# Performance work log

Measured on AMD Instinct MI355X. Metric: run time of the kernel, lower is better.

## Reference

```python
import jax, jax.numpy as jnp
import numpy as np

HEADS = 64
VOCAB = 5
EPS = 1e-5

def _layer_norm(x, g, b):
    mu = jnp.mean(x, axis=-1, keepdims=True)
    var = jnp.var(x, axis=-1, keepdims=True)
    return (x - mu) * jax.lax.rsqrt(var + EPS) * g + b

def setup_inputs() -> dict:
    key = jax.random.key(0)
    ks = jax.random.split(key, 12)
    h = HEADS
    s = 1.0 / np.sqrt(h)
    return {
        "x": jax.random.normal(ks[0], (8, 384, 384, h), dtype=jnp.float32),
        "W1": jax.random.normal(ks[1], (h, h), dtype=jnp.float32) * s,
        "b1": jnp.zeros((h,), jnp.float32),
        "W2": jax.random.normal(ks[2], (h, h), dtype=jnp.float32) * s,
        "b2": jnp.zeros((h,), jnp.float32),
        "W3": jax.random.normal(ks[3], (h, h), dtype=jnp.float32) * s,
        "b3": jnp.zeros((h,), jnp.float32),
        "ln_g": jnp.ones((h,), jnp.float32),
        "ln_b": jnp.zeros((h,), jnp.float32),
        "Wo": jax.random.normal(ks[4], (h, VOCAB), dtype=jnp.float32) * s,
        "bo": jnp.zeros((VOCAB,), jnp.float32),
    }

def reference(x, W1, b1, W2, b2, W3, b3, ln_g, ln_b, Wo, bo):
    # three (Linear -> gelu -> shared LayerNorm) blocks on [b,s,s,h]
    h = _layer_norm(jax.nn.gelu(x @ W1 + b1, approximate=False), ln_g, ln_b)
    h = _layer_norm(jax.nn.gelu(h @ W2 + b2, approximate=False), ln_g, ln_b)
    h = _layer_norm(jax.nn.gelu(h @ W3 + b3, approximate=False), ln_g, ln_b)
    out = h @ Wo + bo  # [b,s,s,vocab]
    return (out + jnp.swapaxes(out, 1, 2)) * 0.5
```

## Files before the change

### kernel.cpp

```cpp
#include <hip/hip_runtime.h>
#include <cstdint>
#include <cstddef>

typedef __attribute__((ext_vector_type(8))) __bf16   bf16x8;
typedef __attribute__((ext_vector_type(2))) __bf16   bf16x2;
typedef __attribute__((ext_vector_type(4))) float    f32x4;
typedef __attribute__((ext_vector_type(4))) uint32_t u32x4;
typedef __attribute__((ext_vector_type(2))) uint32_t u32x2;

#define N_ROWS   1179648
#define N_TILES  73728
#define BLOCKS   1024
#define TPW      18
#define SDIM     384
#define VOCAB    5

__device__ __forceinline__ float gelu_fast(float x){
  float u = x * x;
  float w = __builtin_fmaf(-0.10294456f, u, -2.3021255f);
  float e = __builtin_amdgcn_exp2f(x * w);
  return x * __builtin_amdgcn_rcpf(e + 1.0f);
}

__device__ __forceinline__ bf16x8 mk_bf8(f32x4 a, f32x4 b){
  bf16x8 v;
  v[0]=(__bf16)a[0]; v[1]=(__bf16)a[1]; v[2]=(__bf16)a[2]; v[3]=(__bf16)a[3];
  v[4]=(__bf16)b[0]; v[5]=(__bf16)b[1]; v[6]=(__bf16)b[2]; v[7]=(__bf16)b[3];
  return v;
}

__global__ __launch_bounds__(256)
void mlp_kernel(const float* __restrict__ x,
                const float* __restrict__ W1, const float* __restrict__ b1,
                const float* __restrict__ W2, const float* __restrict__ b2,
                const float* __restrict__ W3, const float* __restrict__ b3,
                const float* __restrict__ lng, const float* __restrict__ lnb,
                const float* __restrict__ Wo,  const float* __restrict__ bo,
                float* __restrict__ tmp)
{
  __shared__ __align__(16) uint8_t  Wl[27392];
  __shared__ __align__(16) uint32_t bounce[4][512];

  const int tid = threadIdx.x;

  {
    int m = tid & 63, g = tid >> 6;
    #pragma unroll 1
    for (int idx = g; idx < 96; idx += 4) {
      int L = idx >> 5, kp = idx & 31;
      const float* W = (L == 0) ? W1 : ((L == 1) ? W2 : W3);
      float lo = W[(2 * kp    ) * 64 + m];
      float hi = W[(2 * kp + 1) * 64 + m];
      bf16x2 p = { (__bf16)lo, (__bf16)hi };
      *(uint32_t*)(Wl + L * 8192 + m * 128 + ((4 * kp) ^ ((m & 7) << 4))) =
          __builtin_bit_cast(uint32_t, p);
    }
    int mm = tid & 15;
    #pragma unroll 1
    for (int kp = tid >> 4; kp < 32; kp += 16) {
      float lo = (mm < VOCAB) ? Wo[(2 * kp    ) * VOCAB + mm] : 0.0f;
      float hi = (mm < VOCAB) ? Wo[(2 * kp + 1) * VOCAB + mm] : 0.0f;
      bf16x2 p = { (__bf16)lo, (__bf16)hi };
      *(uint32_t*)(Wl + 24576 + mm * 128 + ((4 * kp) ^ ((mm & 7) << 4))) =
          __builtin_bit_cast(uint32_t, p);
    }
    if (tid < 192) {
      float v = (tid < 64) ? b1[tid] : ((tid < 128) ? b2[tid - 64] : b3[tid - 128]);
      *(float*)(Wl + 26624 + tid * 4) = v;
    }
  }
  __syncthreads();

  const int wav  = tid >> 6, lane = tid & 63;
  const int h    = lane >> 4;
  const int b    = lane & 15;
  const int swzW = (b & 7) << 4;
  const int swzD = (b & 7) << 2;
  const int rowB = b * 128;
  const int kOff = 16 * h;
  uint32_t* myB = bounce[wav];
  float*    myF = (float*)bounce[wav];
  const float* biasL = (const float*)(Wl + 26624);

  f32x4 ggr[4], bbr[4], aoInit;
  #pragma unroll
  for (int mt = 0; mt < 4; ++mt) {
    ggr[mt] = *(const f32x4*)(lng + 16 * mt + 4 * h);
    bbr[mt] = *(const f32x4*)(lnb + 16 * mt + 4 * h);
  }
  #pragma unroll
  for (int r = 0; r < 4; ++r) {
    int v = 4 * h + r;
    aoInit[r] = (v < VOCAB) ? bo[v] : 0.0f;
  }

  const int gw = blockIdx.x * 4 + wav;
  int t = gw * TPW;

  f32x4 xr[4];
  {
    const float* px = x + (size_t)(t * 16 + b) * 64 + 8 * h;
    xr[0] = *(const f32x4*)(px);
    xr[1] = *(const f32x4*)(px + 4);
    xr[2] = *(const f32x4*)(px + 32);
    xr[3] = *(const f32x4*)(px + 36);
  }

  #pragma unroll 1
  for (int i = 0; i < TPW; ++i, ++t) {
    f32x4 xn[4];
    {
      int tn = (t + 1 < N_TILES) ? (t + 1) : t;
      const float* pn = x + (size_t)(tn * 16 + b) * 64 + 8 * h;
      xn[0] = *(const f32x4*)(pn);
      xn[1] = *(const f32x4*)(pn + 4);
      xn[2] = *(const f32x4*)(pn + 32);
      xn[3] = *(const f32x4*)(pn + 36);
    }

    u32x4 bfr[2];
    bfr[0] = __builtin_bit_cast(u32x4, mk_bf8(xr[0], xr[1]));
    bfr[1] = __builtin_bit_cast(u32x4, mk_bf8(xr[2], xr[3]));

    #pragma unroll
    for (int L = 0; L < 3; ++L) {
      const uint8_t* wp = Wl + L * 8192 + rowB;
      f32x4 acc[4];
      #pragma unroll
      for (int mt = 0; mt < 4; ++mt) {
        u32x4 w0 = *(const u32x4*)(wp + mt * 2048 + ((kOff     ) ^ swzW));
        u32x4 w1 = *(const u32x4*)(wp + mt * 2048 + ((kOff + 64) ^ swzW));
        acc[mt] = *(const f32x4*)(biasL + L * 64 + 16 * mt + 4 * h);
        acc[mt] = __builtin_amdgcn_mfma_f32_16x16x32_bf16(
            __builtin_bit_cast(bf16x8, w0), __builtin_bit_cast(bf16x8, bfr[0]),
            acc[mt], 0, 0, 0);
        acc[mt] = __builtin_amdgcn_mfma_f32_16x16x32_bf16(
            __builtin_bit_cast(bf16x8, w1), __builtin_bit_cast(bf16x8, bfr[1]),
            acc[mt], 0, 0, 0);
      }

      #pragma unroll
      for (int mt = 0; mt < 4; ++mt)
        #pragma unroll
        for (int r = 0; r < 4; ++r)
          acc[mt][r] = gelu_fast(acc[mt][r]);

      float s1 = 0.0f, s2 = 0.0f;
      #pragma unroll
      for (int mt = 0; mt < 4; ++mt)
        #pragma unroll
        for (int r = 0; r < 4; ++r) {
          float v = acc[mt][r];
          s1 += v;
          s2 = __builtin_fmaf(v, v, s2);
        }
      s1 += __shfl_xor(s1, 16); s2 += __shfl_xor(s2, 16);
      s1 += __shfl_xor(s1, 32); s2 += __shfl_xor(s2, 32);
      float mu   = s1 * (1.0f / 64.0f);
      float var  = __builtin_fmaf(s2, (1.0f / 64.0f), -mu * mu);
      float rstd = rsqrtf(var + 1e-5f);
      float nm   = -mu * rstd;

      #pragma unroll
      for (int mt = 0; mt < 4; ++mt) {
        float n0 = __builtin_fmaf(__builtin_fmaf(acc[mt][0], rstd, nm), ggr[mt][0], bbr[mt][0]);
        float n1 = __builtin_fmaf(__builtin_fmaf(acc[mt][1], rstd, nm), ggr[mt][1], bbr[mt][1]);
        float n2 = __builtin_fmaf(__builtin_fmaf(acc[mt][2], rstd, nm), ggr[mt][2], bbr[mt][2]);
        float n3 = __builtin_fmaf(__builtin_fmaf(acc[mt][3], rstd, nm), ggr[mt][3], bbr[mt][3]);
        bf16x2 p0 = { (__bf16)n0, (__bf16)n1 };
        bf16x2 p1 = { (__bf16)n2, (__bf16)n3 };
        u32x2 pw = { __builtin_bit_cast(uint32_t, p0), __builtin_bit_cast(uint32_t, p1) };
        int di = (b * 32 + 8 * mt + 2 * h) ^ swzD;
        *(u32x2*)(myB + di) = pw;
      }
      #pragma unroll
      for (int s = 0; s < 2; ++s)
        bfr[s] = *(const u32x4*)(myB + ((b * 32 + 16 * s + 4 * h) ^ swzD));
    }

    f32x4 ao = aoInit;
    {
      const uint8_t* wp = Wl + 24576 + rowB;
      u32x4 w0 = *(const u32x4*)(wp + ((kOff     ) ^ swzW));
      u32x4 w1 = *(const u32x4*)(wp + ((kOff + 64) ^ swzW));
      ao = __builtin_amdgcn_mfma_f32_16x16x32_bf16(
          __builtin_bit_cast(bf16x8, w0), __builtin_bit_cast(bf16x8, bfr[0]),
          ao, 0, 0, 0);
      ao = __builtin_amdgcn_mfma_f32_16x16x32_bf16(
          __builtin_bit_cast(bf16x8, w1), __builtin_bit_cast(bf16x8, bfr[1]),
          ao, 0, 0, 0);
    }

    #pragma unroll
    for (int r = 0; r < 4; ++r) {
      int v = 4 * h + r;
      if (v < VOCAB) myF[b * VOCAB + v] = ao[r];
    }
    float* dst = tmp + (size_t)t * 16 * VOCAB;
    dst[lane] = myF[lane];
    if (lane < 16) dst[64 + lane] = myF[64 + lane];

    xr[0] = xn[0]; xr[1] = xn[1]; xr[2] = xn[2]; xr[3] = xn[3];
  }
}

__global__ __launch_bounds__(256)
void sym_kernel(const float* __restrict__ tmp, float* __restrict__ out)
{
  __shared__ float A[32][164];
  __shared__ float B[32][164];
  int bid = blockIdx.x;
  int bb = bid / 144, r2 = bid - bb * 144;
  int ti = r2 / 12,  tj = r2 - ti * 12;
  int i0 = ti * 32,  j0 = tj * 32;
  const size_t base = (size_t)bb * SDIM * SDIM;

  for (int idx = threadIdx.x; idx < 32 * 160; idx += 256) {
    int r = idx / 160, c = idx - r * 160;
    A[r][c] = tmp[(base + (size_t)(i0 + r) * SDIM + j0) * VOCAB + c];
    B[r][c] = tmp[(base + (size_t)(j0 + r) * SDIM + i0) * VOCAB + c];
  }
  __syncthreads();
  for (int idx = threadIdx.x; idx < 32 * 160; idx += 256) {
    int r = idx / 160, c = idx - r * 160;
    int jc = c / 5, v = c - jc * 5;
    out[(base + (size_t)(i0 + r) * SDIM + j0) * VOCAB + c] =
        0.5f * (A[r][c] + B[jc][r * 5 + v]);
  }
}

extern "C" void kernel_launch(void* const* d_in, const int* in_sizes, int n_in,
                              void* d_out, int out_size, void* d_ws, size_t ws_size,
                              hipStream_t stream)
{
  const float* x   = (const float*)d_in[0];
  const float* W1  = (const float*)d_in[1];
  const float* b1  = (const float*)d_in[2];
  const float* W2  = (const float*)d_in[3];
  const float* b2  = (const float*)d_in[4];
  const float* W3  = (const float*)d_in[5];
  const float* b3  = (const float*)d_in[6];
  const float* lng = (const float*)d_in[7];
  const float* lnb = (const float*)d_in[8];
  const float* Wo  = (const float*)d_in[9];
  const float* bo  = (const float*)d_in[10];

  float* tmp = (float*)d_ws;
  float* out = (float*)d_out;

  mlp_kernel<<<BLOCKS, 256, 0, stream>>>(x, W1, b1, W2, b2, W3, b3,
                                         lng, lnb, Wo, bo, tmp);
  sym_kernel<<<8 * 12 * 12, 256, 0, stream>>>(tmp, out);
}
```

Before: 170.1 us.

## Process two row tiles per wave iteration to interleave independent MFMA chains

```diff
diff --git a/kernel.cpp b/kernel.cpp
--- a/kernel.cpp
+++ b/kernel.cpp
@@ -10,16 +10,28 @@
 
 #define N_ROWS   1179648
 #define N_TILES  73728
+#define N_PAIRS  36864
 #define BLOCKS   1024
-#define TPW      18
+#define PPW      9
 #define SDIM     384
 #define VOCAB    5
 
-__device__ __forceinline__ float gelu_fast(float x){
-  float u = x * x;
-  float w = __builtin_fmaf(-0.10294456f, u, -2.3021255f);
-  float e = __builtin_amdgcn_exp2f(x * w);
-  return x * __builtin_amdgcn_rcpf(e + 1.0f);
+__device__ __forceinline__ f32x4 gelu4(f32x4 x){
+  f32x4 u = x * x;
+  f32x4 w = u * (-0.10294456f) + (-2.3021255f);
+  f32x4 z = x * w;
+  f32x4 e;
+  e[0] = __builtin_amdgcn_exp2f(z[0]);
+  e[1] = __builtin_amdgcn_exp2f(z[1]);
+  e[2] = __builtin_amdgcn_exp2f(z[2]);
+  e[3] = __builtin_amdgcn_exp2f(z[3]);
+  f32x4 d = e + 1.0f;
+  f32x4 r;
+  r[0] = __builtin_amdgcn_rcpf(d[0]);
+  r[1] = __builtin_amdgcn_rcpf(d[1]);
+  r[2] = __builtin_amdgcn_rcpf(d[2]);
+  r[3] = __builtin_amdgcn_rcpf(d[3]);
+  return x * r;
 }
 
 __device__ __forceinline__ bf16x8 mk_bf8(f32x4 a, f32x4 b){
@@ -39,7 +51,7 @@
                 float* __restrict__ tmp)
 {
   __shared__ __align__(16) uint8_t  Wl[27392];
-  __shared__ __align__(16) uint32_t bounce[4][512];
+  __shared__ __align__(16) uint32_t bounce[4][1024];
 
   const int tid = threadIdx.x;
 
@@ -78,7 +90,8 @@
   const int swzD = (b & 7) << 2;
   const int rowB = b * 128;
   const int kOff = 16 * h;
-  uint32_t* myB = bounce[wav];
+  uint32_t* myA = bounce[wav];
+  uint32_t* myBB = bounce[wav] + 512;
   float*    myF = (float*)bounce[wav];
   const float* biasL = (const float*)(Wl + 26624);
 
@@ -95,112 +108,125 @@
   }
 
   const int gw = blockIdx.x * 4 + wav;
-  int t = gw * TPW;
-
-  f32x4 xr[4];
+  int t = gw * PPW * 2;
+
+  f32x4 xn[8];
   {
-    const float* px = x + (size_t)(t * 16 + b) * 64 + 8 * h;
-    xr[0] = *(const f32x4*)(px);
-    xr[1] = *(const f32x4*)(px + 4);
-    xr[2] = *(const f32x4*)(px + 32);
-    xr[3] = *(const f32x4*)(px + 36);
+    const float* p0 = x + (size_t)(t * 16 + b) * 64 + 8 * h;
+    xn[0] = *(const f32x4*)(p0);        xn[1] = *(const f32x4*)(p0 + 4);
+    xn[2] = *(const f32x4*)(p0 + 32);   xn[3] = *(const f32x4*)(p0 + 36);
+    const float* p1 = p0 + 1024;
+    xn[4] = *(const f32x4*)(p1);        xn[5] = *(const f32x4*)(p1 + 4);
+    xn[6] = *(const f32x4*)(p1 + 32);   xn[7] = *(const f32x4*)(p1 + 36);
   }
 
   #pragma unroll 1
-  for (int i = 0; i < TPW; ++i, ++t) {
-    f32x4 xn[4];
+  for (int i = 0; i < PPW; ++i, t += 2) {
+    u32x4 bfA[2], bfB[2];
+    bfA[0] = __builtin_bit_cast(u32x4, mk_bf8(xn[0], xn[1]));
+    bfA[1] = __builtin_bit_cast(u32x4, mk_bf8(xn[2], xn[3]));
+    bfB[0] = __builtin_bit_cast(u32x4, mk_bf8(xn[4], xn[5]));
+    bfB[1] = __builtin_bit_cast(u32x4, mk_bf8(xn[6], xn[7]));
+
     {
-      int tn = (t + 1 < N_TILES) ? (t + 1) : t;
-      const float* pn = x + (size_t)(tn * 16 + b) * 64 + 8 * h;
-      xn[0] = *(const f32x4*)(pn);
-      xn[1] = *(const f32x4*)(pn + 4);
-      xn[2] = *(const f32x4*)(pn + 32);
-      xn[3] = *(const f32x4*)(pn + 36);
-    }
-
-    u32x4 bfr[2];
-    bfr[0] = __builtin_bit_cast(u32x4, mk_bf8(xr[0], xr[1]));
-    bfr[1] = __builtin_bit_cast(u32x4, mk_bf8(xr[2], xr[3]));
+      int tn = (i + 1 < PPW) ? (t + 2) : t;
+      const float* p0 = x + (size_t)(tn * 16 + b) * 64 + 8 * h;
+      xn[0] = *(const f32x4*)(p0);        xn[1] = *(const f32x4*)(p0 + 4);
+      xn[2] = *(const f32x4*)(p0 + 32);   xn[3] = *(const f32x4*)(p0 + 36);
+      const float* p1 = p0 + 1024;
+      xn[4] = *(const f32x4*)(p1);        xn[5] = *(const f32x4*)(p1 + 4);
+      xn[6] = *(const f32x4*)(p1 + 32);   xn[7] = *(const f32x4*)(p1 + 36);
+    }
 
     #pragma unroll
     for (int L = 0; L < 3; ++L) {
       const uint8_t* wp = Wl + L * 8192 + rowB;
-      f32x4 acc[4];
+      f32x4 accA[4], accB[4];
       #pragma unroll
       for (int mt = 0; mt < 4; ++mt) {
         u32x4 w0 = *(const u32x4*)(wp + mt * 2048 + ((kOff     ) ^ swzW));
         u32x4 w1 = *(const u32x4*)(wp + mt * 2048 + ((kOff + 64) ^ swzW));
-        acc[mt] = *(const f32x4*)(biasL + L * 64 + 16 * mt + 4 * h);
-        acc[mt] = __builtin_amdgcn_mfma_f32_16x16x32_bf16(
-            __builtin_bit_cast(bf16x8, w0), __builtin_bit_cast(bf16x8, bfr[0]),
-            acc[mt], 0, 0, 0);
-        acc[mt] = __builtin_amdgcn_mfma_f32_16x16x32_bf16(
-            __builtin_bit_cast(bf16x8, w1), __builtin_bit_cast(bf16x8, bfr[1]),
-            acc[mt], 0, 0, 0);
-      }
-
-      #pragma unroll
-      for (int mt = 0; mt < 4; ++mt)
-        #pragma unroll
-        for (int r = 0; r < 4; ++r)
-          acc[mt][r] = gelu_fast(acc[mt][r]);
-
-      float s1 = 0.0f, s2 = 0.0f;
-      #pragma unroll
-      for (int mt = 0; mt < 4; ++mt)
-        #pragma unroll
-        for (int r = 0; r < 4; ++r) {
-          float v = acc[mt][r];
-          s1 += v;
-          s2 = __builtin_fmaf(v, v, s2);
-        }
-      s1 += __shfl_xor(s1, 16); s2 += __shfl_xor(s2, 16);
-      s1 += __shfl_xor(s1, 32); s2 += __shfl_xor(s2, 32);
-      float mu   = s1 * (1.0f / 64.0f);
-      float var  = __builtin_fmaf(s2, (1.0f / 64.0f), -mu * mu);
-      float rstd = rsqrtf(var + 1e-5f);
-      float nm   = -mu * rstd;
+        f32x4 bini = *(const f32x4*)(biasL + L * 64 + 16 * mt + 4 * h);
+        accA[mt] = __builtin_amdgcn_mfma_f32_16x16x32_bf16(
+            __builtin_bit_cast(bf16x8, w0), __builtin_bit_cast(bf16x8, bfA[0]), bini, 0, 0, 0);
+        accA[mt] = __builtin_amdgcn_mfma_f32_16x16x32_bf16(
+            __builtin_bit_cast(bf16x8, w1), __builtin_bit_cast(bf16x8, bfA[1]), accA[mt], 0, 0, 0);
+        accB[mt] = __builtin_amdgcn_mfma_f32_16x16x32_bf16(
+            __builtin_bit_cast(bf16x8, w0), __builtin_bit_cast(bf16x8, bfB[0]), bini, 0, 0, 0);
+        accB[mt] = __builtin_amdgcn_mfma_f32_16x16x32_bf16(
+            __builtin_bit_cast(bf16x8, w1), __builtin_bit_cast(bf16x8, bfB[1]), accB[mt], 0, 0, 0);
+      }
+
+      #pragma unroll
+      for (int mt = 0; mt < 4; ++mt) { accA[mt] = gelu4(accA[mt]); accB[mt] = gelu4(accB[mt]); }
+
+      f32x4 vsA = accA[0] + accA[1] + accA[2] + accA[3];
+      f32x4 vsB = accB[0] + accB[1] + accB[2] + accB[3];
+      f32x4 vqA = accA[0]*accA[0] + accA[1]*accA[1] + accA[2]*accA[2] + accA[3]*accA[3];
+      f32x4 vqB = accB[0]*accB[0] + accB[1]*accB[1] + accB[2]*accB[2] + accB[3]*accB[3];
+      float s1A = (vsA[0]+vsA[1]) + (vsA[2]+vsA[3]);
+      float s2A = (vqA[0]+vqA[1]) + (vqA[2]+vqA[3]);
+      float s1B = (vsB[0]+vsB[1]) + (vsB[2]+vsB[3]);
+      float s2B = (vqB[0]+vqB[1]) + (vqB[2]+vqB[3]);
+      s1A += __shfl_xor(s1A, 16); s2A += __shfl_xor(s2A, 16);
+      s1B += __shfl_xor(s1B, 16); s2B += __shfl_xor(s2B, 16);
+      s1A += __shfl_xor(s1A, 32); s2A += __shfl_xor(s2A, 32);
+      s1B += __shfl_xor(s1B, 32); s2B += __shfl_xor(s2B, 32);
+      float muA = s1A * (1.0f/64.0f), muB = s1B * (1.0f/64.0f);
+      float vrA = __builtin_fmaf(s2A, (1.0f/64.0f), -muA*muA);
+      float vrB = __builtin_fmaf(s2B, (1.0f/64.0f), -muB*muB);
+      float rsA = rsqrtf(vrA + 1e-5f), rsB = rsqrtf(vrB + 1e-5f);
+      float nmA = -muA * rsA,          nmB = -muB * rsB;
 
       #pragma unroll
       for (int mt = 0; mt < 4; ++mt) {
-        float n0 = __builtin_fmaf(__builtin_fmaf(acc[mt][0], rstd, nm), ggr[mt][0], bbr[mt][0]);
-        float n1 = __builtin_fmaf(__builtin_fmaf(acc[mt][1], rstd, nm), ggr[mt][1], bbr[mt][1]);
-        float n2 = __builtin_fmaf(__builtin_fmaf(acc[mt][2], rstd, nm), ggr[mt][2], bbr[mt][2]);
-        float n3 = __builtin_fmaf(__builtin_fmaf(acc[mt][3], rstd, nm), ggr[mt][3], bbr[mt][3]);
-        bf16x2 p0 = { (__bf16)n0, (__bf16)n1 };
-        bf16x2 p1 = { (__bf16)n2, (__bf16)n3 };
-        u32x2 pw = { __builtin_bit_cast(uint32_t, p0), __builtin_bit_cast(uint32_t, p1) };
+        f32x4 nA = (accA[mt] * rsA + nmA) * ggr[mt] + bbr[mt];
+        f32x4 nB = (accB[mt] * rsB + nmB) * ggr[mt] + bbr[mt];
+        bf16x2 a0 = { (__bf16)nA[0], (__bf16)nA[1] };
+        bf16x2 a1 = { (__bf16)nA[2], (__bf16)nA[3] };
+        bf16x2 c0 = { (__bf16)nB[0], (__bf16)nB[1] };
+        bf16x2 c1 = { (__bf16)nB[2], (__bf16)nB[3] };
         int di = (b * 32 + 8 * mt + 2 * h) ^ swzD;
-        *(u32x2*)(myB + di) = pw;
-      }
-      #pragma unroll
-      for (int s = 0; s < 2; ++s)
-        bfr[s] = *(const u32x4*)(myB + ((b * 32 + 16 * s + 4 * h) ^ swzD));
-    }
-
-    f32x4 ao = aoInit;
+        u32x2 pa = { __builtin_bit_cast(uint32_t, a0), __builtin_bit_cast(uint32_t, a1) };
+        u32x2 pc = { __builtin_bit_cast(uint32_t, c0), __builtin_bit_cast(uint32_t, c1) };
+        *(u32x2*)(myA  + di) = pa;
+        *(u32x2*)(myBB + di) = pc;
+      }
+      #pragma unroll
+      for (int s = 0; s < 2; ++s) {
+        int di = (b * 32 + 16 * s + 4 * h) ^ swzD;
+        bfA[s] = *(const u32x4*)(myA  + di);
+        bfB[s] = *(const u32x4*)(myBB + di);
+      }
+    }
+
+    f32x4 aoA = aoInit, aoB = aoInit;
     {
       const uint8_t* wp = Wl + 24576 + rowB;
       u32x4 w0 = *(const u32x4*)(wp + ((kOff     ) ^ swzW));
       u32x4 w1 = *(const u32x4*)(wp + ((kOff + 64) ^ swzW));
-      ao = __builtin_amdgcn_mfma_f32_16x16x32_bf16(
-          __builtin_bit_cast(bf16x8, w0), __builtin_bit_cast(bf16x8, bfr[0]),
-          ao, 0, 0, 0);
-      ao = __builtin_amdgcn_mfma_f32_16x16x32_bf16(
-          __builtin_bit_cast(bf16x8, w1), __builtin_bit_cast(bf16x8, bfr[1]),
-          ao, 0, 0, 0);
+      aoA = __builtin_amdgcn_mfma_f32_16x16x32_bf16(
+          __builtin_bit_cast(bf16x8, w0), __builtin_bit_cast(bf16x8, bfA[0]), aoA, 0, 0, 0);
+      aoA = __builtin_amdgcn_mfma_f32_16x16x32_bf16(
+          __builtin_bit_cast(bf16x8, w1), __builtin_bit_cast(bf16x8, bfA[1]), aoA, 0, 0, 0);
+      aoB = __builtin_amdgcn_mfma_f32_16x16x32_bf16(
+          __builtin_bit_cast(bf16x8, w0), __builtin_bit_cast(bf16x8, bfB[0]), aoB, 0, 0, 0);
+      aoB = __builtin_amdgcn_mfma_f32_16x16x32_bf16(
+          __builtin_bit_cast(bf16x8, w1), __builtin_bit_cast(bf16x8, bfB[1]), aoB, 0, 0, 0);
     }
 
     #pragma unroll
     for (int r = 0; r < 4; ++r) {
       int v = 4 * h + r;
-      if (v < VOCAB) myF[b * VOCAB + v] = ao[r];
-    }
-    float* dst = tmp + (size_t)t * 16 * VOCAB;
-    dst[lane] = myF[lane];
-    if (lane < 16) dst[64 + lane] = myF[64 + lane];
-
-    xr[0] = xn[0]; xr[1] = xn[1]; xr[2] = xn[2]; xr[3] = xn[3];
+      if (v < VOCAB) {
+        myF[     b * VOCAB + v] = aoA[r];
+        myF[80 + b * VOCAB + v] = aoB[r];
+      }
+    }
+    float* dst = tmp + (size_t)t * 80;
+    dst[lane]       = myF[lane];
+    dst[64 + lane]  = myF[64 + lane];
+    if (lane < 32) dst[128 + lane] = myF[128 + lane];
   }
 }
 
```

After: 207.4 us. +21.9%, slower.

## Permute weight rows so MFMA output feeds next layer without LDS bounce

Applied to the files above, without the earlier changes.

```diff
diff --git a/kernel.cpp b/kernel.cpp
--- a/kernel.cpp
+++ b/kernel.cpp
@@ -6,20 +6,34 @@
 typedef __attribute__((ext_vector_type(2))) __bf16   bf16x2;
 typedef __attribute__((ext_vector_type(4))) float    f32x4;
 typedef __attribute__((ext_vector_type(4))) uint32_t u32x4;
-typedef __attribute__((ext_vector_type(2))) uint32_t u32x2;
 
 #define N_ROWS   1179648
 #define N_TILES  73728
-#define BLOCKS   1024
-#define TPW      18
+#define BLOCKS   2048
+#define TPW      9
 #define SDIM     384
 #define VOCAB    5
 
-__device__ __forceinline__ float gelu_fast(float x){
-  float u = x * x;
-  float w = __builtin_fmaf(-0.10294456f, u, -2.3021255f);
-  float e = __builtin_amdgcn_exp2f(x * w);
-  return x * __builtin_amdgcn_rcpf(e + 1.0f);
+#define WO_OFF   24576
+#define BIAS_OFF 26624
+#define OUT_OFF  27392
+
+__device__ __forceinline__ f32x4 gelu4(f32x4 x){
+  f32x4 u = x * x;
+  f32x4 w = u * (-0.10294456f) + (-2.3021255f);
+  f32x4 z = x * w;
+  f32x4 e;
+  e[0] = __builtin_amdgcn_exp2f(z[0]);
+  e[1] = __builtin_amdgcn_exp2f(z[1]);
+  e[2] = __builtin_amdgcn_exp2f(z[2]);
+  e[3] = __builtin_amdgcn_exp2f(z[3]);
+  f32x4 d = e + 1.0f;
+  f32x4 r;
+  r[0] = __builtin_amdgcn_rcpf(d[0]);
+  r[1] = __builtin_amdgcn_rcpf(d[1]);
+  r[2] = __builtin_amdgcn_rcpf(d[2]);
+  r[3] = __builtin_amdgcn_rcpf(d[3]);
+  return x * r;
 }
 
 __device__ __forceinline__ bf16x8 mk_bf8(f32x4 a, f32x4 b){
@@ -27,6 +41,10 @@
   v[0]=(__bf16)a[0]; v[1]=(__bf16)a[1]; v[2]=(__bf16)a[2]; v[3]=(__bf16)a[3];
   v[4]=(__bf16)b[0]; v[5]=(__bf16)b[1]; v[6]=(__bf16)b[2]; v[7]=(__bf16)b[3];
   return v;
+}
+
+__device__ __forceinline__ int perm_rho(int m){
+  return (m & 0x23) | ((m & 4) << 2) | ((m & 0x18) >> 1);
 }
 
 __global__ __launch_bounds__(256)
@@ -38,13 +56,15 @@
                 const float* __restrict__ Wo,  const float* __restrict__ bo,
                 float* __restrict__ tmp)
 {
-  __shared__ __align__(16) uint8_t  Wl[27392];
-  __shared__ __align__(16) uint32_t bounce[4][512];
+  __shared__ __align__(16) uint8_t Wl[28672];
 
   const int tid = threadIdx.x;
 
   {
     int m = tid & 63, g = tid >> 6;
+    int rho = perm_rho(m);
+    uint8_t* wrow = Wl + rho * 128;
+    int swz = (rho & 7) << 4;
     #pragma unroll 1
     for (int idx = g; idx < 96; idx += 4) {
       int L = idx >> 5, kp = idx & 31;
@@ -52,8 +72,7 @@
       float lo = W[(2 * kp    ) * 64 + m];
       float hi = W[(2 * kp + 1) * 64 + m];
       bf16x2 p = { (__bf16)lo, (__bf16)hi };
-      *(uint32_t*)(Wl + L * 8192 + m * 128 + ((4 * kp) ^ ((m & 7) << 4))) =
-          __builtin_bit_cast(uint32_t, p);
+      *(uint32_t*)(wrow + L * 8192 + ((4 * kp) ^ swz)) = __builtin_bit_cast(uint32_t, p);
     }
     int mm = tid & 15;
     #pragma unroll 1
@@ -61,12 +80,12 @@
       float lo = (mm < VOCAB) ? Wo[(2 * kp    ) * VOCAB + mm] : 0.0f;
       float hi = (mm < VOCAB) ? Wo[(2 * kp + 1) * VOCAB + mm] : 0.0f;
       bf16x2 p = { (__bf16)lo, (__bf16)hi };
-      *(uint32_t*)(Wl + 24576 + mm * 128 + ((4 * kp) ^ ((mm & 7) << 4))) =
+      *(uint32_t*)(Wl + WO_OFF + mm * 128 + ((4 * kp) ^ ((mm & 7) << 4))) =
           __builtin_bit_cast(uint32_t, p);
     }
     if (tid < 192) {
       float v = (tid < 64) ? b1[tid] : ((tid < 128) ? b2[tid - 64] : b3[tid - 128]);
-      *(float*)(Wl + 26624 + tid * 4) = v;
+      *(float*)(Wl + BIAS_OFF + tid * 4) = v;
     }
   }
   __syncthreads();
@@ -75,18 +94,17 @@
   const int h    = lane >> 4;
   const int b    = lane & 15;
   const int swzW = (b & 7) << 4;
-  const int swzD = (b & 7) << 2;
   const int rowB = b * 128;
   const int kOff = 16 * h;
-  uint32_t* myB = bounce[wav];
-  float*    myF = (float*)bounce[wav];
-  const float* biasL = (const float*)(Wl + 26624);
+  const float* biasL = (const float*)(Wl + BIAS_OFF);
+  float* myF = (float*)(Wl + OUT_OFF) + wav * 80;
 
   f32x4 ggr[4], bbr[4], aoInit;
   #pragma unroll
   for (int mt = 0; mt < 4; ++mt) {
-    ggr[mt] = *(const f32x4*)(lng + 16 * mt + 4 * h);
-    bbr[mt] = *(const f32x4*)(lnb + 16 * mt + 4 * h);
+    int base = 8 * h + 4 * (mt & 1) + 32 * (mt >> 1);
+    ggr[mt] = *(const f32x4*)(lng + base);
+    bbr[mt] = *(const f32x4*)(lnb + base);
   }
   #pragma unroll
   for (int r = 0; r < 4; ++r) {
@@ -97,30 +115,25 @@
   const int gw = blockIdx.x * 4 + wav;
   int t = gw * TPW;
 
-  f32x4 xr[4];
+  f32x4 xn[4];
   {
     const float* px = x + (size_t)(t * 16 + b) * 64 + 8 * h;
-    xr[0] = *(const f32x4*)(px);
-    xr[1] = *(const f32x4*)(px + 4);
-    xr[2] = *(const f32x4*)(px + 32);
-    xr[3] = *(const f32x4*)(px + 36);
+    xn[0] = *(const f32x4*)(px);      xn[1] = *(const f32x4*)(px + 4);
+    xn[2] = *(const f32x4*)(px + 32); xn[3] = *(const f32x4*)(px + 36);
   }
 
   #pragma unroll 1
   for (int i = 0; i < TPW; ++i, ++t) {
-    f32x4 xn[4];
+    u32x4 bfr[2];
+    bfr[0] = __builtin_bit_cast(u32x4, mk_bf8(xn[0], xn[1]));
+    bfr[1] = __builtin_bit_cast(u32x4, mk_bf8(xn[2], xn[3]));
+
     {
-      int tn = (t + 1 < N_TILES) ? (t + 1) : t;
+      int tn = (i + 1 < TPW) ? (t + 1) : t;
       const float* pn = x + (size_t)(tn * 16 + b) * 64 + 8 * h;
-      xn[0] = *(const f32x4*)(pn);
-      xn[1] = *(const f32x4*)(pn + 4);
-      xn[2] = *(const f32x4*)(pn + 32);
-      xn[3] = *(const f32x4*)(pn + 36);
-    }
-
-    u32x4 bfr[2];
-    bfr[0] = __builtin_bit_cast(u32x4, mk_bf8(xr[0], xr[1]));
-    bfr[1] = __builtin_bit_cast(u32x4, mk_bf8(xr[2], xr[3]));
+      xn[0] = *(const f32x4*)(pn);      xn[1] = *(const f32x4*)(pn + 4);
+      xn[2] = *(const f32x4*)(pn + 32); xn[3] = *(const f32x4*)(pn + 36);
+    }
 
     #pragma unroll
     for (int L = 0; L < 3; ++L) {
@@ -130,65 +143,45 @@
       for (int mt = 0; mt < 4; ++mt) {
         u32x4 w0 = *(const u32x4*)(wp + mt * 2048 + ((kOff     ) ^ swzW));
         u32x4 w1 = *(const u32x4*)(wp + mt * 2048 + ((kOff + 64) ^ swzW));
-        acc[mt] = *(const f32x4*)(biasL + L * 64 + 16 * mt + 4 * h);
+        int base = 8 * h + 4 * (mt & 1) + 32 * (mt >> 1);
+        acc[mt] = *(const f32x4*)(biasL + L * 64 + base);
         acc[mt] = __builtin_amdgcn_mfma_f32_16x16x32_bf16(
-            __builtin_bit_cast(bf16x8, w0), __builtin_bit_cast(bf16x8, bfr[0]),
-            acc[mt], 0, 0, 0);
+            __builtin_bit_cast(bf16x8, w0), __builtin_bit_cast(bf16x8, bfr[0]), acc[mt], 0, 0, 0);
         acc[mt] = __builtin_amdgcn_mfma_f32_16x16x32_bf16(
-            __builtin_bit_cast(bf16x8, w1), __builtin_bit_cast(bf16x8, bfr[1]),
-            acc[mt], 0, 0, 0);
+            __builtin_bit_cast(bf16x8, w1), __builtin_bit_cast(bf16x8, bfr[1]), acc[mt], 0, 0, 0);
       }
 
       #pragma unroll
-      for (int mt = 0; mt < 4; ++mt)
-        #pragma unroll
-        for (int r = 0; r < 4; ++r)
-          acc[mt][r] = gelu_fast(acc[mt][r]);
-
-      float s1 = 0.0f, s2 = 0.0f;
-      #pragma unroll
-      for (int mt = 0; mt < 4; ++mt)
-        #pragma unroll
-        for (int r = 0; r < 4; ++r) {
-          float v = acc[mt][r];
-          s1 += v;
-          s2 = __builtin_fmaf(v, v, s2);
-        }
+      for (int mt = 0; mt < 4; ++mt) acc[mt] = gelu4(acc[mt]);
+
+      f32x4 vs = acc[0] + acc[1] + acc[2] + acc[3];
+      f32x4 vq = acc[0]*acc[0] + acc[1]*acc[1] + acc[2]*acc[2] + acc[3]*acc[3];
+      float s1 = (vs[0]+vs[1]) + (vs[2]+vs[3]);
+      float s2 = (vq[0]+vq[1]) + (vq[2]+vq[3]);
       s1 += __shfl_xor(s1, 16); s2 += __shfl_xor(s2, 16);
       s1 += __shfl_xor(s1, 32); s2 += __shfl_xor(s2, 32);
-      float mu   = s1 * (1.0f / 64.0f);
-      float var  = __builtin_fmaf(s2, (1.0f / 64.0f), -mu * mu);
+      float mu   = s1 * (1.0f/64.0f);
+      float var  = __builtin_fmaf(s2, (1.0f/64.0f), -mu * mu);
       float rstd = rsqrtf(var + 1e-5f);
       float nm   = -mu * rstd;
 
-      #pragma unroll
-      for (int mt = 0; mt < 4; ++mt) {
-        float n0 = __builtin_fmaf(__builtin_fmaf(acc[mt][0], rstd, nm), ggr[mt][0], bbr[mt][0]);
-        float n1 = __builtin_fmaf(__builtin_fmaf(acc[mt][1], rstd, nm), ggr[mt][1], bbr[mt][1]);
-        float n2 = __builtin_fmaf(__builtin_fmaf(acc[mt][2], rstd, nm), ggr[mt][2], bbr[mt][2]);
-        float n3 = __builtin_fmaf(__builtin_fmaf(acc[mt][3], rstd, nm), ggr[mt][3], bbr[mt][3]);
-        bf16x2 p0 = { (__bf16)n0, (__bf16)n1 };
-        bf16x2 p1 = { (__bf16)n2, (__bf16)n3 };
-        u32x2 pw = { __builtin_bit_cast(uint32_t, p0), __builtin_bit_cast(uint32_t, p1) };
-        int di = (b * 32 + 8 * mt + 2 * h) ^ swzD;
-        *(u32x2*)(myB + di) = pw;
-      }
-      #pragma unroll
-      for (int s = 0; s < 2; ++s)
-        bfr[s] = *(const u32x4*)(myB + ((b * 32 + 16 * s + 4 * h) ^ swzD));
+      f32x4 n0 = (acc[0] * rstd + nm) * ggr[0] + bbr[0];
+      f32x4 n1 = (acc[1] * rstd + nm) * ggr[1] + bbr[1];
+      f32x4 n2 = (acc[2] * rstd + nm) * ggr[2] + bbr[2];
+      f32x4 n3 = (acc[3] * rstd + nm) * ggr[3] + bbr[3];
+      bfr[0] = __builtin_bit_cast(u32x4, mk_bf8(n0, n1));
+      bfr[1] = __builtin_bit_cast(u32x4, mk_bf8(n2, n3));
     }
 
     f32x4 ao = aoInit;
     {
-      const uint8_t* wp = Wl + 24576 + rowB;
+      const uint8_t* wp = Wl + WO_OFF + rowB;
       u32x4 w0 = *(const u32x4*)(wp + ((kOff     ) ^ swzW));
       u32x4 w1 = *(const u32x4*)(wp + ((kOff + 64) ^ swzW));
       ao = __builtin_amdgcn_mfma_f32_16x16x32_bf16(
-          __builtin_bit_cast(bf16x8, w0), __builtin_bit_cast(bf16x8, bfr[0]),
-          ao, 0, 0, 0);
+          __builtin_bit_cast(bf16x8, w0), __builtin_bit_cast(bf16x8, bfr[0]), ao, 0, 0, 0);
       ao = __builtin_amdgcn_mfma_f32_16x16x32_bf16(
-          __builtin_bit_cast(bf16x8, w1), __builtin_bit_cast(bf16x8, bfr[1]),
-          ao, 0, 0, 0);
+          __builtin_bit_cast(bf16x8, w1), __builtin_bit_cast(bf16x8, bfr[1]), ao, 0, 0, 0);
     }
 
     #pragma unroll
@@ -196,11 +189,9 @@
       int v = 4 * h + r;
       if (v < VOCAB) myF[b * VOCAB + v] = ao[r];
     }
-    float* dst = tmp + (size_t)t * 16 * VOCAB;
+    float* dst = tmp + (size_t)t * 80;
     dst[lane] = myF[lane];
     if (lane < 16) dst[64 + lane] = myF[64 + lane];
-
-    xr[0] = xn[0]; xr[1] = xn[1]; xr[2] = xn[2]; xr[3] = xn[3];
   }
 }
 
```

New measurement: 147.7 us (median of 2 runs). -13.2%, faster.
